# Optimization experiments

Hardware: AMD Instinct MI355X
Metric: run time of the kernel (lower is better)

Reference implementation:

```python
import jax, jax.numpy as jnp
import numpy as np

VOCAB = 200000
EDIM = 256
R = 16


def setup_inputs() -> dict:
    key = jax.random.key(0)
    k0, k1, k2 = jax.random.split(key, 3)
    x = jax.random.randint(k0, (4096, 50), 0, VOCAB)
    # TR cores: core0 (r1, num_embeddings, r0), core1 (r0, embedding_dim, r1)
    core0 = jax.random.normal(k1, (R, VOCAB, R), dtype=jnp.float32)
    core1 = jax.random.normal(k2, (R, EDIM, R), dtype=jnp.float32)
    return {"x": x, "core0": core0, "core1": core1}


def reference(x, core0, core1):
    # tr_to_tensor for 2 cores: weight[i, j] = trace(core0[:, i, :] @ core1[:, j, :])
    # core0: (a=r1, i=vocab, b=r0), core1: (b=r0, j=edim, a=r1)
    weight = jnp.einsum('aib,bja->ij', core0, core1)  # [vocab, edim]
    return weight[x]  # gather: [batch, hist, edim]
```

## Files before the change

### kernel.cpp

```cpp
#include <hip/hip_runtime.h>
#include <hip/hip_bf16.h>

#define VOCAB 200000
#define EDIM  256

typedef __attribute__((ext_vector_type(4))) float  f32x4;
typedef __attribute__((ext_vector_type(8))) __bf16 bf16x8;

__device__ __forceinline__ __bf16 f2bf(float f) {
    unsigned u = __builtin_bit_cast(unsigned, f);
    u += 0x7FFFu + ((u >> 16) & 1u);
    unsigned short s = (unsigned short)(u >> 16);
    return __builtin_bit_cast(__bf16, s);
}

__global__ void pack_b_kernel(const float* __restrict__ core1, bf16x8* __restrict__ bpk) {
    int t    = blockIdx.x * 256 + threadIdx.x;
    int lane = t & 63;
    int nt   = (t >> 6) & 15;
    int kk   = t >> 10;
    int j     = nt * 16 + (lane & 15);
    int kbase = kk * 32 + ((lane >> 4) * 8);
    bf16x8 v;
#pragma unroll
    for (int e = 0; e < 8; ++e) {
        int k = kbase + e;
        int b = k & 15, a = k >> 4;
        v[e] = f2bf(core1[(b * 256 + j) * 16 + a]);
    }
    bpk[t] = v;
}

__global__ __launch_bounds__(512, 4) void tr_embed_kernel(
        const int* __restrict__ x, const float* __restrict__ core0,
        const bf16x8* __restrict__ bpk, float* __restrict__ out) {
    __shared__ bf16x8 smem[4096];
    const int tid  = threadIdx.x;
    const int lane = tid & 63;
    const int wave = tid >> 6;

    const int xcd  = blockIdx.x & 7;
    const int slot = blockIdx.x >> 3;
    const int rowTile = xcd * 200 + (slot >> 1);
    const int colHalf = slot & 1;

    const int rowBase = rowTile * 128 + wave * 16;
    const int idx = x[rowBase + (lane & 15)];

#pragma unroll
    for (int i = 0; i < 8; ++i) {
        int e   = i * 512 + tid;
        int kk  = e >> 9;
        int ntl = (e >> 6) & 7;
        int ln  = e & 63;
        smem[e] = bpk[(kk * 16 + colHalf * 8 + ntl) * 64 + ln];
    }

    const int half = lane >> 4;
    const float* aptr = core0 + ((long)(half >> 1) * VOCAB + idx) * 16 + (half & 1) * 8;
    const int KST = 2 * VOCAB * 16;

    f32x4 pa[8], pb[8];
#pragma unroll
    for (int k = 0; k < 8; ++k) {
        pa[k] = *(const f32x4*)(aptr + (long)k * KST);
        pb[k] = *(const f32x4*)(aptr + (long)k * KST + 4);
    }

    __syncthreads();

    f32x4 acc[8] = {};
#pragma unroll
    for (int kk = 0; kk < 8; ++kk) {
        bf16x8 af;
#pragma unroll
        for (int e = 0; e < 4; ++e) { af[e] = f2bf(pa[kk][e]); af[e + 4] = f2bf(pb[kk][e]); }

        const bf16x8* bs = smem + kk * 512 + lane;
#pragma unroll
        for (int ntl = 0; ntl < 8; ++ntl)
            acc[ntl] = __builtin_amdgcn_mfma_f32_16x16x32_bf16(af, bs[ntl * 64], acc[ntl], 0, 0, 0);
    }

    float* obase = out + (long)rowBase * 256 + colHalf * 128 + (lane & 15);
#pragma unroll
    for (int ntl = 0; ntl < 8; ++ntl) {
#pragma unroll
        for (int e = 0; e < 4; ++e) {
            obase[(half * 4 + e) * 256 + ntl * 16] = acc[ntl][e];
        }
    }
}

extern "C" void kernel_launch(void* const* d_in, const int* in_sizes, int n_in,
                              void* d_out, int out_size, void* d_ws, size_t ws_size,
                              hipStream_t stream) {
    const int*   x     = (const int*)d_in[0];
    const float* core0 = (const float*)d_in[1];
    const float* core1 = (const float*)d_in[2];
    float* out = (float*)d_out;
    bf16x8* bpk = (bf16x8*)d_ws;

    pack_b_kernel<<<32, 256, 0, stream>>>(core1, bpk);
    tr_embed_kernel<<<3200, 512, 0, stream>>>(x, core0, bpk, out);
}
```

Measured before the change: 132.2 us.

## Process both column halves per block to reuse gathered A rows, use LDS direct loads

Each block now handles a full 256-column row tile, so it computes both column halves in sequence instead of splitting them across two blocks. The gathered core0 rows and their bf16 conversion are done once and reused for both halves, which halves the random gather traffic. B tiles are staged into LDS with global_load_lds direct loads, and the grid is halved, dropping the XCD-aware block remapping. The cost is an extra pair of barriers, serialized B reloads inside each block, and fewer blocks available to hide latency.

```diff
diff --git a/kernel.cpp b/kernel.cpp
--- a/kernel.cpp
+++ b/kernel.cpp
@@ -6,6 +6,9 @@
 
 typedef __attribute__((ext_vector_type(4))) float  f32x4;
 typedef __attribute__((ext_vector_type(8))) __bf16 bf16x8;
+
+typedef const __attribute__((address_space(1))) unsigned int* gas_u32p;
+typedef __attribute__((address_space(3))) unsigned int* las_u32p;
 
 __device__ __forceinline__ __bf16 f2bf(float f) {
     unsigned u = __builtin_bit_cast(unsigned, f);
@@ -39,56 +42,78 @@
     const int lane = tid & 63;
     const int wave = tid >> 6;
 
-    const int xcd  = blockIdx.x & 7;
-    const int slot = blockIdx.x >> 3;
-    const int rowTile = xcd * 200 + (slot >> 1);
-    const int colHalf = slot & 1;
+    const int rowBase = blockIdx.x * 128 + wave * 16;
+    const int idx = x[rowBase + (lane & 15)];
 
-    const int rowBase = rowTile * 128 + wave * 16;
-    const int idx = x[rowBase + (lane & 15)];
+    const int half = lane >> 4;
+    const float* aptr = core0 + ((long)(half >> 1) * VOCAB + idx) * 16 + (half & 1) * 8;
+    const long KST = 2L * VOCAB * 16;
 
 #pragma unroll
     for (int i = 0; i < 8; ++i) {
-        int e   = i * 512 + tid;
-        int kk  = e >> 9;
-        int ntl = (e >> 6) & 7;
-        int ln  = e & 63;
-        smem[e] = bpk[(kk * 16 + colHalf * 8 + ntl) * 64 + ln];
+        const bf16x8* src = bpk + (i * 16 + 0 * 8 + wave) * 64 + lane;
+        __builtin_amdgcn_global_load_lds((gas_u32p)src, (las_u32p)(smem + i * 512 + wave * 64),
+                                         16, 0, 0);
     }
-
-    const int half = lane >> 4;
-    const float* aptr = core0 + ((long)(half >> 1) * VOCAB + idx) * 16 + (half & 1) * 8;
-    const int KST = 2 * VOCAB * 16;
 
     f32x4 pa[8], pb[8];
 #pragma unroll
     for (int k = 0; k < 8; ++k) {
-        pa[k] = *(const f32x4*)(aptr + (long)k * KST);
-        pb[k] = *(const f32x4*)(aptr + (long)k * KST + 4);
+        pa[k] = *(const f32x4*)(aptr + k * KST);
+        pb[k] = *(const f32x4*)(aptr + k * KST + 4);
+    }
+    bf16x8 af[8];
+#pragma unroll
+    for (int k = 0; k < 8; ++k) {
+#pragma unroll
+        for (int e = 0; e < 4; ++e) { af[k][e] = f2bf(pa[k][e]); af[k][e + 4] = f2bf(pb[k][e]); }
     }
 
     __syncthreads();
 
-    f32x4 acc[8] = {};
+    float* obase = out + (long)rowBase * 256 + (lane & 15);
+
+    {
+        f32x4 acc[8] = {};
 #pragma unroll
-    for (int kk = 0; kk < 8; ++kk) {
-        bf16x8 af;
+        for (int kk = 0; kk < 8; ++kk) {
+            const bf16x8* bs = smem + kk * 512 + lane;
 #pragma unroll
-        for (int e = 0; e < 4; ++e) { af[e] = f2bf(pa[kk][e]); af[e + 4] = f2bf(pb[kk][e]); }
-
-        const bf16x8* bs = smem + kk * 512 + lane;
+            for (int ntl = 0; ntl < 8; ++ntl)
+                acc[ntl] = __builtin_amdgcn_mfma_f32_16x16x32_bf16(af[kk], bs[ntl * 64], acc[ntl], 0, 0, 0);
+        }
 #pragma unroll
         for (int ntl = 0; ntl < 8; ++ntl)
-            acc[ntl] = __builtin_amdgcn_mfma_f32_16x16x32_bf16(af, bs[ntl * 64], acc[ntl], 0, 0, 0);
+#pragma unroll
+            for (int e = 0; e < 4; ++e)
+                obase[(half * 4 + e) * 256 + ntl * 16] = acc[ntl][e];
     }
 
-    float* obase = out + (long)rowBase * 256 + colHalf * 128 + (lane & 15);
+    __syncthreads();
+
 #pragma unroll
-    for (int ntl = 0; ntl < 8; ++ntl) {
+    for (int i = 0; i < 8; ++i) {
+        const bf16x8* src = bpk + (i * 16 + 8 + wave) * 64 + lane;
+        __builtin_amdgcn_global_load_lds((gas_u32p)src, (las_u32p)(smem + i * 512 + wave * 64),
+                                         16, 0, 0);
+    }
+
+    __syncthreads();
+
+    {
+        f32x4 acc[8] = {};
 #pragma unroll
-        for (int e = 0; e < 4; ++e) {
-            obase[(half * 4 + e) * 256 + ntl * 16] = acc[ntl][e];
+        for (int kk = 0; kk < 8; ++kk) {
+            const bf16x8* bs = smem + kk * 512 + lane;
+#pragma unroll
+            for (int ntl = 0; ntl < 8; ++ntl)
+                acc[ntl] = __builtin_amdgcn_mfma_f32_16x16x32_bf16(af[kk], bs[ntl * 64], acc[ntl], 0, 0, 0);
         }
+#pragma unroll
+        for (int ntl = 0; ntl < 8; ++ntl)
+#pragma unroll
+            for (int e = 0; e < 4; ++e)
+                obase[(half * 4 + e) * 256 + 128 + ntl * 16] = acc[ntl][e];
     }
 }
 
@@ -102,5 +127,5 @@
     bf16x8* bpk = (bf16x8*)d_ws;
 
     pack_b_kernel<<<32, 256, 0, stream>>>(core1, bpk);
-    tr_embed_kernel<<<3200, 512, 0, stream>>>(x, core0, bpk, out);
+    tr_embed_kernel<<<1600, 512, 0, stream>>>(x, core0, bpk, out);
 }
```

Measured after the change: 121.2 us. 1.09x faster.

## Switch to persistent blocks with atomic work queue and full-width B in LDS

Applied to the files above, without the earlier changes.

Replaces the 3200-block grid with 256 persistent 1024-thread blocks. Each block loads the whole packed B matrix into LDS once, using direct global-to-LDS loads. Each wave then pulls 16-row tiles from a global atomic counter and computes all 256 output columns per tile. This is meant to avoid reloading B per block and to stop gathering the same core0 rows twice for the two column halves. In exchange it adds an atomic per tile, 128KB of LDS per block, and a larger accumulator register footprint, which may reduce occupancy and latency hiding.

```diff
diff --git a/kernel.cpp b/kernel.cpp
--- a/kernel.cpp
+++ b/kernel.cpp
@@ -3,9 +3,13 @@
 
 #define VOCAB 200000
 #define EDIM  256
+#define NTILES 12800
 
 typedef __attribute__((ext_vector_type(4))) float  f32x4;
 typedef __attribute__((ext_vector_type(8))) __bf16 bf16x8;
+
+typedef const __attribute__((address_space(1))) unsigned int* gas_u32p;
+typedef __attribute__((address_space(3))) unsigned int* las_u32p;
 
 __device__ __forceinline__ __bf16 f2bf(float f) {
     unsigned u = __builtin_bit_cast(unsigned, f);
@@ -14,7 +18,9 @@
     return __builtin_bit_cast(__bf16, s);
 }
 
-__global__ void pack_b_kernel(const float* __restrict__ core1, bf16x8* __restrict__ bpk) {
+__global__ void pack_b_kernel(const float* __restrict__ core1, bf16x8* __restrict__ bpk,
+                              unsigned* __restrict__ counter) {
+    if (blockIdx.x == 0 && threadIdx.x == 0) *counter = 0u;
     int t    = blockIdx.x * 256 + threadIdx.x;
     int lane = t & 63;
     int nt   = (t >> 6) & 15;
@@ -31,64 +37,67 @@
     bpk[t] = v;
 }
 
-__global__ __launch_bounds__(512, 4) void tr_embed_kernel(
+__global__ __launch_bounds__(1024, 4) void tr_embed_kernel(
         const int* __restrict__ x, const float* __restrict__ core0,
-        const bf16x8* __restrict__ bpk, float* __restrict__ out) {
-    __shared__ bf16x8 smem[4096];
+        const bf16x8* __restrict__ bpk, unsigned* __restrict__ counter,
+        float* __restrict__ out) {
+    __shared__ bf16x8 smem[8192];
     const int tid  = threadIdx.x;
     const int lane = tid & 63;
     const int wave = tid >> 6;
 
-    const int xcd  = blockIdx.x & 7;
-    const int slot = blockIdx.x >> 3;
-    const int rowTile = xcd * 200 + (slot >> 1);
-    const int colHalf = slot & 1;
-
-    const int rowBase = rowTile * 128 + wave * 16;
-    const int idx = x[rowBase + (lane & 15)];
-
 #pragma unroll
     for (int i = 0; i < 8; ++i) {
-        int e   = i * 512 + tid;
-        int kk  = e >> 9;
-        int ntl = (e >> 6) & 7;
-        int ln  = e & 63;
-        smem[e] = bpk[(kk * 16 + colHalf * 8 + ntl) * 64 + ln];
+        const bf16x8* src = bpk + i * 1024 + tid;
+        __builtin_amdgcn_global_load_lds((gas_u32p)src,
+                                         (las_u32p)(smem + i * 1024 + wave * 64), 16, 0, 0);
     }
 
     const int half = lane >> 4;
-    const float* aptr = core0 + ((long)(half >> 1) * VOCAB + idx) * 16 + (half & 1) * 8;
-    const int KST = 2 * VOCAB * 16;
-
-    f32x4 pa[8], pb[8];
-#pragma unroll
-    for (int k = 0; k < 8; ++k) {
-        pa[k] = *(const f32x4*)(aptr + (long)k * KST);
-        pb[k] = *(const f32x4*)(aptr + (long)k * KST + 4);
-    }
+    const int col  = lane & 15;
+    const long KST = 2L * VOCAB * 16;
 
     __syncthreads();
 
-    f32x4 acc[8] = {};
+    for (;;) {
+        int t = 0;
+        if (lane == 0) t = (int)atomicAdd(counter, 1u);
+        t = __builtin_amdgcn_readfirstlane(t);
+        if (t >= NTILES) break;
+
+        const int rowBase = t * 16;
+        const int idx = x[rowBase + col];
+        const float* aptr = core0 + ((long)(half >> 1) * VOCAB + idx) * 16 + (half & 1) * 8;
+
+        f32x4 pa[8], pb[8];
 #pragma unroll
-    for (int kk = 0; kk < 8; ++kk) {
-        bf16x8 af;
+        for (int k = 0; k < 8; ++k) {
+            pa[k] = *(const f32x4*)(aptr + k * KST);
+            pb[k] = *(const f32x4*)(aptr + k * KST + 4);
+        }
+        __builtin_amdgcn_sched_barrier(0);
+
+        bf16x8 af[8];
 #pragma unroll
-        for (int e = 0; e < 4; ++e) { af[e] = f2bf(pa[kk][e]); af[e + 4] = f2bf(pb[kk][e]); }
+        for (int k = 0; k < 8; ++k)
+#pragma unroll
+            for (int e = 0; e < 4; ++e) { af[k][e] = f2bf(pa[k][e]); af[k][e + 4] = f2bf(pb[k][e]); }
 
-        const bf16x8* bs = smem + kk * 512 + lane;
+        f32x4 acc[16] = {};
 #pragma unroll
-        for (int ntl = 0; ntl < 8; ++ntl)
-            acc[ntl] = __builtin_amdgcn_mfma_f32_16x16x32_bf16(af, bs[ntl * 64], acc[ntl], 0, 0, 0);
-    }
+        for (int kk = 0; kk < 8; ++kk) {
+            const bf16x8* bs = smem + kk * 1024 + lane;
+#pragma unroll
+            for (int nt = 0; nt < 16; ++nt)
+                acc[nt] = __builtin_amdgcn_mfma_f32_16x16x32_bf16(af[kk], bs[nt * 64], acc[nt], 0, 0, 0);
+        }
 
-    float* obase = out + (long)rowBase * 256 + colHalf * 128 + (lane & 15);
+        float* obase = out + (long)rowBase * 256 + col;
 #pragma unroll
-    for (int ntl = 0; ntl < 8; ++ntl) {
+        for (int nt = 0; nt < 16; ++nt)
 #pragma unroll
-        for (int e = 0; e < 4; ++e) {
-            obase[(half * 4 + e) * 256 + ntl * 16] = acc[ntl][e];
-        }
+            for (int e = 0; e < 4; ++e)
+                obase[(half * 4 + e) * 256 + nt * 16] = acc[nt][e];
     }
 }
 
@@ -99,8 +108,9 @@
     const float* core0 = (const float*)d_in[1];
     const float* core1 = (const float*)d_in[2];
     float* out = (float*)d_out;
-    bf16x8* bpk = (bf16x8*)d_ws;
+    bf16x8*   bpk     = (bf16x8*)d_ws;
+    unsigned* counter = (unsigned*)((char*)d_ws + 131072);
 
-    pack_b_kernel<<<32, 256, 0, stream>>>(core1, bpk);
-    tr_embed_kernel<<<3200, 512, 0, stream>>>(x, core0, bpk, out);
+    pack_b_kernel<<<32, 256, 0, stream>>>(core1, bpk, counter);
+    tr_embed_kernel<<<256, 1024, 0, stream>>>(x, core0, bpk, counter, out);
 }
```

Result: slower. 230.3 us (+74.2%).

## Stage core0 gathers and B tiles into LDS via direct global-to-LDS loads

Applied to the files above, without the earlier changes.

Replaces the register-held core0 gathers and register-staged B copy with direct global_load_lds transfers into shared memory. Each wave's 16 gathered rows are laid out in an XOR-swizzled pattern so each lane loads a contiguous 1KB row, then fragments are read back from LDS. Blocks shrink to 256 threads and 64 rows with twice as many blocks. The aim is fewer vector registers and more memory parallelism, at the cost of 128KB of LDS per block, which caps occupancy at one block per CU, plus extra LDS read traffic.

```diff
diff --git a/kernel.cpp b/kernel.cpp
--- a/kernel.cpp
+++ b/kernel.cpp
@@ -6,6 +6,9 @@
 
 typedef __attribute__((ext_vector_type(4))) float  f32x4;
 typedef __attribute__((ext_vector_type(8))) __bf16 bf16x8;
+
+typedef const __attribute__((address_space(1))) unsigned int* gas_u32p;
+typedef __attribute__((address_space(3))) unsigned int* las_u32p;
 
 __device__ __forceinline__ __bf16 f2bf(float f) {
     unsigned u = __builtin_bit_cast(unsigned, f);
@@ -31,65 +34,69 @@
     bpk[t] = v;
 }
 
-__global__ __launch_bounds__(512, 4) void tr_embed_kernel(
+__global__ __launch_bounds__(256) void tr_embed_kernel(
         const int* __restrict__ x, const float* __restrict__ core0,
         const bf16x8* __restrict__ bpk, float* __restrict__ out) {
-    __shared__ bf16x8 smem[4096];
+    __shared__ f32x4 smem4[8192];
+    char* const base = (char*)smem4;
     const int tid  = threadIdx.x;
     const int lane = tid & 63;
     const int wave = tid >> 6;
 
     const int xcd  = blockIdx.x & 7;
     const int slot = blockIdx.x >> 3;
-    const int rowTile = xcd * 200 + (slot >> 1);
+    const int rowTile = xcd * 400 + (slot >> 1);
     const int colHalf = slot & 1;
 
-    const int rowBase = rowTile * 128 + wave * 16;
-    const int idx = x[rowBase + (lane & 15)];
+    const int rowBase = rowTile * 64 + wave * 16;
+    const int myidx = x[rowBase + (lane & 15)];
 
 #pragma unroll
-    for (int i = 0; i < 8; ++i) {
-        int e   = i * 512 + tid;
-        int kk  = e >> 9;
-        int ntl = (e >> 6) & 7;
-        int ln  = e & 63;
-        smem[e] = bpk[(kk * 16 + colHalf * 8 + ntl) * 64 + ln];
+    for (int i = 0; i < 16; ++i) {
+        int rb  = wave * 16 + i;
+        int kk  = rb >> 3, ntl = rb & 7;
+        const bf16x8* src = bpk + (kk * 16 + colHalf * 8 + ntl) * 64 + lane;
+        __builtin_amdgcn_global_load_lds((gas_u32p)src, (las_u32p)(base + rb * 1024), 16, 0, 0);
     }
 
-    const int half = lane >> 4;
-    const float* aptr = core0 + ((long)(half >> 1) * VOCAB + idx) * 16 + (half & 1) * 8;
-    const int KST = 2 * VOCAB * 16;
-
-    f32x4 pa[8], pb[8];
+    char* const awave = base + 65536 + wave * 16384;
 #pragma unroll
-    for (int k = 0; k < 8; ++k) {
-        pa[k] = *(const f32x4*)(aptr + (long)k * KST);
-        pb[k] = *(const f32x4*)(aptr + (long)k * KST + 4);
+    for (int r = 0; r < 16; ++r) {
+        int idxr = __builtin_amdgcn_readlane(myidx, r);
+        int g = lane ^ (r & 7);
+        const float* src = core0 + ((long)(g >> 2) * VOCAB + idxr) * 16 + (g & 3) * 4;
+        __builtin_amdgcn_global_load_lds((gas_u32p)src, (las_u32p)(awave + r * 1024), 16, 0, 0);
     }
 
     __syncthreads();
 
+    const int q = lane >> 4;
+    const int s = lane & 7;
+    const char* ab = awave + (lane & 15) * 1024;
     f32x4 acc[8] = {};
 #pragma unroll
     for (int kk = 0; kk < 8; ++kk) {
+        int c0 = kk * 8 + q * 2;
+        f32x4 lo = *(const f32x4*)(ab + ((c0 ^ s) << 4));
+        f32x4 hi = *(const f32x4*)(ab + (((c0 + 1) ^ s) << 4));
         bf16x8 af;
 #pragma unroll
-        for (int e = 0; e < 4; ++e) { af[e] = f2bf(pa[kk][e]); af[e + 4] = f2bf(pb[kk][e]); }
+        for (int e = 0; e < 4; ++e) { af[e] = f2bf(lo[e]); af[e + 4] = f2bf(hi[e]); }
 
-        const bf16x8* bs = smem + kk * 512 + lane;
+        const char* bb = base + kk * 8192 + lane * 16;
 #pragma unroll
-        for (int ntl = 0; ntl < 8; ++ntl)
-            acc[ntl] = __builtin_amdgcn_mfma_f32_16x16x32_bf16(af, bs[ntl * 64], acc[ntl], 0, 0, 0);
+        for (int ntl = 0; ntl < 8; ++ntl) {
+            bf16x8 bfr = *(const bf16x8*)(bb + ntl * 1024);
+            acc[ntl] = __builtin_amdgcn_mfma_f32_16x16x32_bf16(af, bfr, acc[ntl], 0, 0, 0);
+        }
     }
 
     float* obase = out + (long)rowBase * 256 + colHalf * 128 + (lane & 15);
 #pragma unroll
-    for (int ntl = 0; ntl < 8; ++ntl) {
+    for (int ntl = 0; ntl < 8; ++ntl)
 #pragma unroll
-        for (int e = 0; e < 4; ++e) {
-            obase[(half * 4 + e) * 256 + ntl * 16] = acc[ntl][e];
-        }
-    }
+        for (int e = 0; e < 4; ++e)
+            obase[(q * 4 + e) * 256 + ntl * 16] = acc[ntl][e];
 }
 
 extern "C" void kernel_launch(void* const* d_in, const int* in_sizes, int n_in,
@@ -102,5 +109,5 @@
     bf16x8* bpk = (bf16x8*)d_ws;
 
     pack_b_kernel<<<32, 256, 0, stream>>>(core1, bpk);
-    tr_embed_kernel<<<3200, 512, 0, stream>>>(x, core0, bpk, out);
+    tr_embed_kernel<<<6400, 256, 0, stream>>>(x, core0, bpk, out);
 }
```

Measured after the change: 176.8 us. 33.7% more time.
